# Performance work log

Measured on AMD Instinct MI355X. Metric: run time of the kernel, lower is better.

Reference implementation:

```python
import jax, jax.numpy as jnp
import numpy as np

C, H, W = 32, 64, 64
KH, KW = 5, 5
OH, OW = 60, 60
N_IN = C * H * W
B, S = 64, 4096
CAP = 128


def _build_indices():
    # Enumerate every (c, kh, kw, oh, ow) slot of the unfold, matching
    # fold(unfold(order)) in the torch module (stride 1, pad 0, dilation 1).
    c = np.arange(C)[:, None, None, None, None]
    kh = np.arange(KH)[None, :, None, None, None]
    kw = np.arange(KW)[None, None, :, None, None]
    oh = np.arange(OH)[None, None, None, :, None]
    ow = np.arange(OW)[None, None, None, None, :]
    ids = c * (H * W) + (oh + kh) * W + (ow + kw)          # input flat id feeding slot
    ckk = c * (KH * KW) + kh * KW + kw                     # kernel-local channel index
    j = ckk * (OH * OW) + oh * OW + ow                     # flat slot in order_convoled
    ids, j = np.broadcast_arrays(ids, j)
    ids = ids.ravel().astype(np.int64)
    j = j.ravel().astype(np.int64)
    perm = np.argsort(ids, kind='stable')
    sid, sj = ids[perm], j[perm]
    counts = np.bincount(ids, minlength=N_IN)
    Lmax = int(counts.max())                               # = 25 here
    starts = np.concatenate([[0], np.cumsum(counts)[:-1]])
    rank = np.arange(sid.shape[0]) - starts[sid]
    indices = np.full((N_IN, Lmax), -1, dtype=np.int32)
    indices[sid, rank] = sj
    return indices


def setup_inputs() -> dict:
    key = jax.random.key(0)
    spikes = jax.random.randint(key, (B, S, 1, 1), 0, N_IN, dtype=jnp.int32)
    indices = jnp.asarray(_build_indices())
    return {"spikes": spikes, "indices": indices, "out_h": OH, "out_w": OW, "cap": CAP}


def reference(spikes, indices, out_h, out_w, cap):
    Bn, Sn = spikes.shape[0], spikes.shape[1]
    L = indices.shape[1]
    nbins = out_h * out_w
    E = Sn * L                                             # events per batch element

    ids = spikes[:, :, 0, 0]                               # [B,S] flat input ids
    g = indices[ids]                                       # [B,S,L] slots, -1 padded
    valid = g >= 0
    j = jnp.where(valid, g, 0)
    bins = (j % nbins).reshape(Bn * E)                     # output bin (oh*out_w+ow)
    ckk = (j // nbins).reshape(Bn * E)                     # kernel-local index to store
    valid_f = valid.reshape(Bn * E)
    b_idx = jnp.repeat(jnp.arange(Bn, dtype=jnp.int32), E)

    # Arrival-order rank within each (batch, bin): stable sort by global bin,
    # then rank = position - segment start (running max of change points).
    gbin = jnp.where(valid_f, b_idx * nbins + bins, Bn * nbins)   # sentinel for invalid
    perm = jnp.argsort(gbin)                               # stable
    sorted_gbin = gbin[perm]
    pos = jnp.arange(Bn * E, dtype=jnp.int32)
    change = jnp.concatenate([jnp.ones((1,), bool), sorted_gbin[1:] != sorted_gbin[:-1]])
    seg_start = jax.lax.cummax(jnp.where(change, pos, 0))
    rank_sorted = pos - seg_start
    rank = jnp.zeros(Bn * E, jnp.int32).at[perm].set(rank_sorted)  # inverse perm

    # Scatter ckk into per-bin slots; invalid / overflow events go to slot=cap (dropped).
    slot = jnp.where(valid_f & (rank < cap), rank, cap)
    out = jnp.full((Bn, cap + 1, nbins), -1, dtype=spikes.dtype)
    out = out.at[b_idx, slot, bins].set(jnp.where(valid_f, ckk, -1), mode='drop')
    return out[:, :cap].reshape(Bn, cap, out_h, out_w)
```

## Files before the change

### kernel.cpp

```cpp
#include <hip/hip_runtime.h>

#define OHh   60
#define OWw   60
#define NBINS (OHh * OWw)
#define NB    64
#define NS    4096
#define CAP   128

#define NW     4
#define SEG    (NS / NW)
#define CH     (SEG / 64)
#define WSLOTS 40
#define PRE0   64

__global__ __launch_bounds__(256) void sort_spikes_row4(
    const int* __restrict__ spikes, int* __restrict__ out) {
    const int bid  = (int)blockIdx.x;
    const int b    = bid & (NB - 1);
    const int row  = bid >> 6;
    const int tid  = (int)threadIdx.x;
    const int wv   = tid >> 6;
    const int lane = tid & 63;
    const bool valid  = lane < OWw;
    const int  lane_c = valid ? lane : 127;

    __shared__ short          stage[NW][WSLOTS + 1][64];
    __shared__ unsigned short hits[NW][64];
    __shared__ int            cnt[NW][64];
    __shared__ int            ovf;

    if (tid == 0) ovf = 0;

    const int* __restrict__ sp   = spikes + b * NS + wv * SEG;
    int* __restrict__       outb = out + (size_t)b * (CAP * NBINS) + row * OWw;

    int vs[CH];
#pragma unroll
    for (int c = 0; c < CH; ++c) vs[c] = sp[c * 64 + lane];

    unsigned short* const hitbuf      = &hits[wv][0];
    short* const          stage_lane  = &stage[wv][0][lane];
    short* const          stage_dummy = &stage[wv][WSLOTS][lane];

    int count = 0;
#pragma unroll
    for (int c = 0; c < CH; ++c) {
        const int v   = vs[c];
        const int kh  = ((v >> 6) & 63) - row;
        const bool halo = (unsigned)kh < 5u;
        const int w   = v & 63;
        const int A   = (v >> 12) * 25 + kh * 5 + w;
        const unsigned short P = (unsigned short)((w << 10) | A);

        const unsigned long long mask = __ballot(halo);
        const int pos = __builtin_amdgcn_mbcnt_hi(
            (unsigned)(mask >> 32),
            __builtin_amdgcn_mbcnt_lo((unsigned)mask, 0));
        if (halo) hitbuf[pos] = P;
        const int n = __popcll(mask);

        for (int i = 0; i < n; ++i) {
            const int Pj  = (int)hitbuf[i];
            const int kw  = (Pj >> 10) - lane_c;
            const bool inwin = (unsigned)kw < 5u;
            const int val = (Pj & 0x3ff) - lane_c;
            short* a = (inwin & (count < WSLOTS))
                           ? (stage_lane + count * 64)
                           : stage_dummy;
            *a = (short)val;
            count += inwin;
        }

        if (valid) outb[(PRE0 + wv * CH + c) * NBINS + lane] = -1;
    }
    cnt[wv][lane] = count;
    if (__ballot(count > WSLOTS) && lane == 0) ovf = 1;
    __syncthreads();

    if (ovf == 0) {
        if (valid) {
            const int c0 = cnt[0][lane], c1 = cnt[1][lane];
            const int c2 = cnt[2][lane], c3 = cnt[3][lane];
            const int o1 = c0, o2 = c0 + c1, o3 = o2 + c2;
            const int total = o3 + c3;
#pragma unroll 4
            for (int i = 0; i < PRE0 / NW; ++i) {
                const int k = wv * (PRE0 / NW) + i;
                int val = -1;
                if (k < total) {
                    int wsel = 0, base = 0;
                    if (k >= o1) { wsel = 1; base = o1; }
                    if (k >= o2) { wsel = 2; base = o2; }
                    if (k >= o3) { wsel = 3; base = o3; }
                    val = (int)stage[wsel][k - base][lane];
                }
                outb[k * NBINS + lane] = val;
            }
            for (int k = PRE0 + wv; k < total && k < CAP; k += NW) {
                int wsel = 0, base = 0;
                if (k >= o1) { wsel = 1; base = o1; }
                if (k >= o2) { wsel = 2; base = o2; }
                if (k >= o3) { wsel = 3; base = o3; }
                outb[k * NBINS + lane] = (int)stage[wsel][k - base][lane];
            }
        }
    } else if (wv == 0) {
        const int* __restrict__ spf = spikes + b * NS;
        int cc = 0;
        for (int c = 0; c < NS / 64; ++c) {
            const int v = spf[c * 64 + lane];
            const int h = (v >> 6) & 63;
            unsigned long long mask = __ballot((unsigned)(h - row) < 5u);
            while (mask) {
                const int j = (int)__builtin_ctzll(mask);
                mask &= mask - 1;
                const int vj =
                    __builtin_amdgcn_readlane(v, __builtin_amdgcn_readfirstlane(j));
                const int wj  = vj & 63;
                const int khj = ((vj >> 6) & 63) - row;
                const int cj  = vj >> 12;
                const int kw  = wj - lane;
                if (((unsigned)kw < 5u) & valid) {
                    if (cc < CAP)
                        outb[cc * NBINS + lane] = cj * 25 + khj * 5 + kw;
                    ++cc;
                }
            }
        }
        if (valid)
            for (int k = cc; k < CAP; ++k) outb[k * NBINS + lane] = -1;
    }
}

extern "C" void kernel_launch(void* const* d_in, const int* in_sizes, int n_in,
                              void* d_out, int out_size, void* d_ws, size_t ws_size,
                              hipStream_t stream) {
    const int* spikes = (const int*)d_in[0];
    int* out = (int*)d_out;

    dim3 grid(OHh * NB);
    dim3 block(256);
    sort_spikes_row4<<<grid, block, 0, stream>>>(spikes, out);
}
```

Baseline: 148.9 us.

## Accumulate halo hits then scatter to bins with ballot-based match-any ranking

Each wave now collects all halo hits for its segment into a shared buffer first. It then processes them 12 at a time, with each lane taking one (hit, kw) pair, instead of every lane scanning every hit serially per chunk. Per-bin ranks come from a six-ballot match-any over the bin id, and the stage layout becomes bin-major. This cuts the serial per-hit loop by roughly a factor of 12. In exchange it adds a hit-buffer cap with overflow fallback and a smaller per-bin staging capacity, so the slow fallback path may trigger more often.

```diff
diff --git a/kernel.cpp b/kernel.cpp
--- a/kernel.cpp
+++ b/kernel.cpp
@@ -10,8 +10,10 @@
 #define NW     4
 #define SEG    (NS / NW)
 #define CH     (SEG / 64)
-#define WSLOTS 40
+#define WSLOTS 32
 #define PRE0   64
+#define HCAP   176
+#define HSINK  192
 
 __global__ __launch_bounds__(256) void sort_spikes_row4(
     const int* __restrict__ spikes, int* __restrict__ out) {
@@ -21,15 +23,15 @@
     const int tid  = (int)threadIdx.x;
     const int wv   = tid >> 6;
     const int lane = tid & 63;
-    const bool valid  = lane < OWw;
-    const int  lane_c = valid ? lane : 127;
+    const bool valid = lane < OWw;
 
-    __shared__ short          stage[NW][WSLOTS + 1][64];
-    __shared__ unsigned short hits[NW][64];
-    __shared__ int            cnt[NW][64];
-    __shared__ int            ovf;
+    __shared__ short stage[NW][64][WSLOTS + 1];
+    __shared__ __align__(8) unsigned short hits[NW][256];
+    __shared__ int   cnt[NW][64];
+    __shared__ int   ovf;
 
     if (tid == 0) ovf = 0;
+    cnt[wv][lane] = 0;
 
     const int* __restrict__ sp   = spikes + b * NS + wv * SEG;
     int* __restrict__       outb = out + (size_t)b * (CAP * NBINS) + row * OWw;
@@ -38,43 +40,67 @@
 #pragma unroll
     for (int c = 0; c < CH; ++c) vs[c] = sp[c * 64 + lane];
 
-    unsigned short* const hitbuf      = &hits[wv][0];
-    short* const          stage_lane  = &stage[wv][0][lane];
-    short* const          stage_dummy = &stage[wv][WSLOTS][lane];
+    unsigned short* const hitbuf = &hits[wv][0];
+    const int sinkw = HSINK + lane;
 
-    int count = 0;
+    int hbase = 0;
 #pragma unroll
     for (int c = 0; c < CH; ++c) {
-        const int v   = vs[c];
-        const int kh  = ((v >> 6) & 63) - row;
+        const int v  = vs[c];
+        const int kh = ((v >> 6) & 63) - row;
         const bool halo = (unsigned)kh < 5u;
-        const int w   = v & 63;
-        const int A   = (v >> 12) * 25 + kh * 5 + w;
-        const unsigned short P = (unsigned short)((w << 10) | A);
+        const unsigned short P =
+            (unsigned short)(((v & 63) << 8) | ((v >> 12) << 3) | (kh & 7));
 
         const unsigned long long mask = __ballot(halo);
         const int pos = __builtin_amdgcn_mbcnt_hi(
             (unsigned)(mask >> 32),
             __builtin_amdgcn_mbcnt_lo((unsigned)mask, 0));
-        if (halo) hitbuf[pos] = P;
-        const int n = __popcll(mask);
-
-        for (int i = 0; i < n; ++i) {
-            const int Pj  = (int)hitbuf[i];
-            const int kw  = (Pj >> 10) - lane_c;
-            const bool inwin = (unsigned)kw < 5u;
-            const int val = (Pj & 0x3ff) - lane_c;
-            short* a = (inwin & (count < WSLOTS))
-                           ? (stage_lane + count * 64)
-                           : stage_dummy;
-            *a = (short)val;
-            count += inwin;
-        }
+        const int idx = halo ? (hbase + pos) : sinkw;
+        hitbuf[idx] = P;
+        hbase = min(hbase + (int)__popcll(mask), HCAP);
 
         if (valid) outb[(PRE0 + wv * CH + c) * NBINS + lane] = -1;
     }
-    cnt[wv][lane] = count;
-    if (__ballot(count > WSLOTS) && lane == 0) ovf = 1;
+    if (hbase >= HCAP && lane == 0) ovf = 1;
+
+    const int qi  = (lane < 60) ? (lane / 5) : 4096;
+    const int kwc = lane - qi * 5;
+
+    const int n = hbase;
+    short* const stg = &stage[wv][0][0];
+    int*   const cw  = &cnt[wv][0];
+    for (int hb = 0; hb < n; hb += 12) {
+        const int  hidx = hb + qi;
+        const bool hv   = hidx < n;
+        const int  ridx = hv ? hidx : sinkw;
+        const unsigned P = hitbuf[ridx];
+        const int  w    = (int)(P >> 8);
+        const int  bin  = w - kwc;
+        const bool ok   = hv & ((unsigned)bin < 60u);
+        const int  route = ok ? bin : 62;
+        const int  val  = ((int)((P >> 3) & 31)) * 25 + ((int)(P & 7)) * 5 + kwc;
+
+        unsigned long long m = ~0ull;
+#pragma unroll
+        for (int t = 0; t < 6; ++t) {
+            const bool bit = (route >> t) & 1;
+            const unsigned long long bb = __ballot(bit);
+            m &= bit ? bb : ~bb;
+        }
+        const int rank = __builtin_amdgcn_mbcnt_hi(
+            (unsigned)(m >> 32), __builtin_amdgcn_mbcnt_lo((unsigned)m, 0));
+        const int tot  = (int)__popcll(m);
+        const int base = cw[route];
+        const int slot = min(base + rank, WSLOTS);
+        stg[route * (WSLOTS + 1) + slot] = (short)val;
+        if (rank == tot - 1) cw[route] = base + tot;
+    }
+
+    {
+        const int mycnt = cw[lane];
+        if (__ballot(mycnt > WSLOTS) && lane == 0) ovf = 1;
+    }
     __syncthreads();
 
     if (ovf == 0) {
@@ -92,7 +118,7 @@
                     if (k >= o1) { wsel = 1; base = o1; }
                     if (k >= o2) { wsel = 2; base = o2; }
                     if (k >= o3) { wsel = 3; base = o3; }
-                    val = (int)stage[wsel][k - base][lane];
+                    val = (int)stage[wsel][lane][k - base];
                 }
                 outb[k * NBINS + lane] = val;
             }
@@ -101,7 +127,7 @@
                 if (k >= o1) { wsel = 1; base = o1; }
                 if (k >= o2) { wsel = 2; base = o2; }
                 if (k >= o3) { wsel = 3; base = o3; }
-                outb[k * NBINS + lane] = (int)stage[wsel][k - base][lane];
+                outb[k * NBINS + lane] = (int)stage[wsel][lane][k - base];
             }
         }
     } else if (wv == 0) {
```

Result: slower. 277.5 us (+86.3%).

## Process two output rows per block with two waves per row

Applied to the files above, without the earlier changes.

Each block now handles a pair of output rows. Two waves serve each row, and each wave scans half the spike stream (2048 spikes, loaded in two chunks of 16) instead of a quarter. This halves the grid and the number of redundant spike loads, and makes the merge step choose between only two staged buffers. In exchange, each wave has a serial hit-processing chain twice as long, and the fixed 40-slot staging buffer is more likely to overflow into the slow fallback path.

```diff
diff --git a/kernel.cpp b/kernel.cpp
--- a/kernel.cpp
+++ b/kernel.cpp
@@ -8,21 +8,28 @@
 #define CAP   128
 
 #define NW     4
-#define SEG    (NS / NW)
+#define RPB    2
+#define RG     (OHh / RPB)
+#define SEGS   2
+#define SEG    (NS / SEGS)
 #define CH     (SEG / 64)
 #define WSLOTS 40
 #define PRE0   64
 
-__global__ __launch_bounds__(256) void sort_spikes_row4(
+__global__ __launch_bounds__(256) void sort_spikes_rowpair(
     const int* __restrict__ spikes, int* __restrict__ out) {
     const int bid  = (int)blockIdx.x;
     const int b    = bid & (NB - 1);
-    const int row  = bid >> 6;
+    const int rg   = bid >> 6;
     const int tid  = (int)threadIdx.x;
     const int wv   = tid >> 6;
     const int lane = tid & 63;
     const bool valid  = lane < OWw;
     const int  lane_c = valid ? lane : 127;
+
+    const int rsub = wv >> 1;
+    const int seg  = wv & 1;
+    const int row  = rg * RPB + rsub;
 
     __shared__ short          stage[NW][WSLOTS + 1][64];
     __shared__ unsigned short hits[NW][64];
@@ -31,12 +38,8 @@
 
     if (tid == 0) ovf = 0;
 
-    const int* __restrict__ sp   = spikes + b * NS + wv * SEG;
+    const int* __restrict__ sp   = spikes + b * NS + seg * SEG;
     int* __restrict__       outb = out + (size_t)b * (CAP * NBINS) + row * OWw;
-
-    int vs[CH];
-#pragma unroll
-    for (int c = 0; c < CH; ++c) vs[c] = sp[c * 64 + lane];
 
     unsigned short* const hitbuf      = &hits[wv][0];
     short* const          stage_lane  = &stage[wv][0][lane];
@@ -44,34 +47,42 @@
 
     int count = 0;
 #pragma unroll
-    for (int c = 0; c < CH; ++c) {
-        const int v   = vs[c];
-        const int kh  = ((v >> 6) & 63) - row;
-        const bool halo = (unsigned)kh < 5u;
-        const int w   = v & 63;
-        const int A   = (v >> 12) * 25 + kh * 5 + w;
-        const unsigned short P = (unsigned short)((w << 10) | A);
+    for (int half = 0; half < 2; ++half) {
+        int vs[16];
+#pragma unroll
+        for (int c = 0; c < 16; ++c) vs[c] = sp[(half * 16 + c) * 64 + lane];
 
-        const unsigned long long mask = __ballot(halo);
-        const int pos = __builtin_amdgcn_mbcnt_hi(
-            (unsigned)(mask >> 32),
-            __builtin_amdgcn_mbcnt_lo((unsigned)mask, 0));
-        if (halo) hitbuf[pos] = P;
-        const int n = __popcll(mask);
+#pragma unroll
+        for (int c = 0; c < 16; ++c) {
+            const int cc  = half * 16 + c;
+            const int v   = vs[c];
+            const int kh  = ((v >> 6) & 63) - row;
+            const bool halo = (unsigned)kh < 5u;
+            const int w   = v & 63;
+            const int A   = (v >> 12) * 25 + kh * 5 + w;
+            const unsigned short P = (unsigned short)((w << 10) | A);
 
-        for (int i = 0; i < n; ++i) {
-            const int Pj  = (int)hitbuf[i];
-            const int kw  = (Pj >> 10) - lane_c;
-            const bool inwin = (unsigned)kw < 5u;
-            const int val = (Pj & 0x3ff) - lane_c;
-            short* a = (inwin & (count < WSLOTS))
-                           ? (stage_lane + count * 64)
-                           : stage_dummy;
-            *a = (short)val;
-            count += inwin;
+            const unsigned long long mask = __ballot(halo);
+            const int pos = __builtin_amdgcn_mbcnt_hi(
+                (unsigned)(mask >> 32),
+                __builtin_amdgcn_mbcnt_lo((unsigned)mask, 0));
+            if (halo) hitbuf[pos] = P;
+            const int n = __popcll(mask);
+
+            for (int i = 0; i < n; ++i) {
+                const int Pj  = (int)hitbuf[i];
+                const int kw  = (Pj >> 10) - lane_c;
+                const bool inwin = (unsigned)kw < 5u;
+                const int val = (Pj & 0x3ff) - lane_c;
+                short* a = (inwin & (count < WSLOTS))
+                               ? (stage_lane + count * 64)
+                               : stage_dummy;
+                *a = (short)val;
+                count += inwin;
+            }
+
+            if (valid) outb[(PRE0 + seg * CH + cc) * NBINS + lane] = -1;
         }
-
-        if (valid) outb[(PRE0 + wv * CH + c) * NBINS + lane] = -1;
     }
     cnt[wv][lane] = count;
     if (__ballot(count > WSLOTS) && lane == 0) ovf = 1;
@@ -79,32 +90,28 @@
 
     if (ovf == 0) {
         if (valid) {
-            const int c0 = cnt[0][lane], c1 = cnt[1][lane];
-            const int c2 = cnt[2][lane], c3 = cnt[3][lane];
-            const int o1 = c0, o2 = c0 + c1, o3 = o2 + c2;
-            const int total = o3 + c3;
+            const int w0 = rsub * SEGS;
+            const int c0 = cnt[w0][lane], c1 = cnt[w0 + 1][lane];
+            const int total = c0 + c1;
+            const int kbase = seg * 32;
 #pragma unroll 4
-            for (int i = 0; i < PRE0 / NW; ++i) {
-                const int k = wv * (PRE0 / NW) + i;
+            for (int i = 0; i < 32; ++i) {
+                const int k = kbase + i;
                 int val = -1;
                 if (k < total) {
-                    int wsel = 0, base = 0;
-                    if (k >= o1) { wsel = 1; base = o1; }
-                    if (k >= o2) { wsel = 2; base = o2; }
-                    if (k >= o3) { wsel = 3; base = o3; }
+                    const int wsel = (k >= c0) ? (w0 + 1) : w0;
+                    const int base = (k >= c0) ? c0 : 0;
                     val = (int)stage[wsel][k - base][lane];
                 }
                 outb[k * NBINS + lane] = val;
             }
-            for (int k = PRE0 + wv; k < total && k < CAP; k += NW) {
-                int wsel = 0, base = 0;
-                if (k >= o1) { wsel = 1; base = o1; }
-                if (k >= o2) { wsel = 2; base = o2; }
-                if (k >= o3) { wsel = 3; base = o3; }
+            for (int k = PRE0 + seg; k < total && k < CAP; k += SEGS) {
+                const int wsel = (k >= c0) ? (w0 + 1) : w0;
+                const int base = (k >= c0) ? c0 : 0;
                 outb[k * NBINS + lane] = (int)stage[wsel][k - base][lane];
             }
         }
-    } else if (wv == 0) {
+    } else if (seg == 0) {
         const int* __restrict__ spf = spikes + b * NS;
         int cc = 0;
         for (int c = 0; c < NS / 64; ++c) {
@@ -138,7 +145,7 @@
     const int* spikes = (const int*)d_in[0];
     int* out = (int*)d_out;
 
-    dim3 grid(OHh * NB);
+    dim3 grid(RG * NB);
     dim3 block(256);
-    sort_spikes_row4<<<grid, block, 0, stream>>>(spikes, out);
+    sort_spikes_rowpair<<<grid, block, 0, stream>>>(spikes, out);
 }
```

Result: slower. 153.6 us (+3.1%).

## Replace per-hit lane broadcast loop with atomic presence bitmasks per bin

Applied to the files above, without the earlier changes.

Each wave now appends all halo hits to a shared buffer with up to 160 entries, instead of replaying every hit across all lanes. Lanes are grouped so that each group of five scatters one hit's five kernel-width taps into per-bin presence bitmasks using shared-memory atomicOr, twelve hits per pass. Each bin then walks its own bitmask in arrival order and writes into a shared output image, which is copied out to global memory in coalesced rows. The aim is to cut the serial n-iteration loop that every lane ran per chunk. In exchange the kernel adds LDS atomics, an extra block barrier and a larger shared footprint, and the bitmask walk is divergent across lanes.

```diff
diff --git a/kernel.cpp b/kernel.cpp
--- a/kernel.cpp
+++ b/kernel.cpp
@@ -10,7 +10,7 @@
 #define NW     4
 #define SEG    (NS / NW)
 #define CH     (SEG / 64)
-#define WSLOTS 40
+#define HCAP   160
 #define PRE0   64
 
 __global__ __launch_bounds__(256) void sort_spikes_row4(
@@ -21,15 +21,22 @@
     const int tid  = (int)threadIdx.x;
     const int wv   = tid >> 6;
     const int lane = tid & 63;
-    const bool valid  = lane < OWw;
-    const int  lane_c = valid ? lane : 127;
+    const bool valid = lane < OWw;
 
-    __shared__ short          stage[NW][WSLOTS + 1][64];
-    __shared__ unsigned short hits[NW][64];
+    __shared__ int            hitbuf[NW][256];
+    __shared__ unsigned       pres[NW][64][7];
+    __shared__ unsigned short outimg[PRE0][OWw];
     __shared__ int            cnt[NW][64];
     __shared__ int            ovf;
 
     if (tid == 0) ovf = 0;
+#pragma unroll
+    for (int i = 0; i < 5; ++i) pres[wv][lane][i] = 0u;
+
+    {
+        int* oi = (int*)&outimg[0][0];
+        for (int i = tid; i < PRE0 * OWw / 2; i += 256) oi[i] = -1;
+    }
 
     const int* __restrict__ sp   = spikes + b * NS + wv * SEG;
     int* __restrict__       outb = out + (size_t)b * (CAP * NBINS) + row * OWw;
@@ -38,70 +45,75 @@
 #pragma unroll
     for (int c = 0; c < CH; ++c) vs[c] = sp[c * 64 + lane];
 
-    unsigned short* const hitbuf      = &hits[wv][0];
-    short* const          stage_lane  = &stage[wv][0][lane];
-    short* const          stage_dummy = &stage[wv][WSLOTS][lane];
+    int* const hb_w = &hitbuf[wv][0];
+    const int row5 = row * 5;
 
-    int count = 0;
+    int hbase = 0;
 #pragma unroll
     for (int c = 0; c < CH; ++c) {
-        const int v   = vs[c];
-        const int kh  = ((v >> 6) & 63) - row;
-        const bool halo = (unsigned)kh < 5u;
-        const int w   = v & 63;
-        const int A   = (v >> 12) * 25 + kh * 5 + w;
-        const unsigned short P = (unsigned short)((w << 10) | A);
+        const int v = vs[c];
+        const int h = (v >> 6) & 63;
+        const int w = v & 63;
+        const int A = (v >> 12) * 25 + h * 5 + w - row5;
+        const int R = (w << 16) | A;
+        const bool halo = (unsigned)(h - row) < 5u;
 
         const unsigned long long mask = __ballot(halo);
         const int pos = __builtin_amdgcn_mbcnt_hi(
             (unsigned)(mask >> 32),
             __builtin_amdgcn_mbcnt_lo((unsigned)mask, 0));
-        if (halo) hitbuf[pos] = P;
-        const int n = __popcll(mask);
-
-        for (int i = 0; i < n; ++i) {
-            const int Pj  = (int)hitbuf[i];
-            const int kw  = (Pj >> 10) - lane_c;
-            const bool inwin = (unsigned)kw < 5u;
-            const int val = (Pj & 0x3ff) - lane_c;
-            short* a = (inwin & (count < WSLOTS))
-                           ? (stage_lane + count * 64)
-                           : stage_dummy;
-            *a = (short)val;
-            count += inwin;
-        }
+        if (halo) hb_w[min(hbase + pos, 255)] = R;
+        hbase += (int)__popcll(mask);
 
         if (valid) outb[(PRE0 + wv * CH + c) * NBINS + lane] = -1;
     }
-    cnt[wv][lane] = count;
-    if (__ballot(count > WSLOTS) && lane == 0) ovf = 1;
+    if (hbase > HCAP && lane == 0) ovf = 1;
+    const int n = min(hbase, HCAP);
+
+    const int qi  = (lane < OWw) ? (lane / 5) : 4096;
+    const int kwc = lane - qi * 5;
+    for (int hbi = 0; hbi < n; hbi += 12) {
+        const int hidx = hbi + qi;
+        const int R    = hb_w[min(hidx, 255)];
+        const int bin  = (R >> 16) - kwc;
+        if (((unsigned)bin < 60u) && (hidx < n)) {
+            atomicOr(&pres[wv][bin][hidx >> 5], 1u << (hidx & 31));
+        }
+    }
+
+    unsigned m0 = pres[wv][lane][0], m1 = pres[wv][lane][1];
+    unsigned m2 = pres[wv][lane][2], m3 = pres[wv][lane][3];
+    unsigned m4 = pres[wv][lane][4];
+    cnt[wv][lane] = __builtin_popcount(m0) + __builtin_popcount(m1) +
+                    __builtin_popcount(m2) + __builtin_popcount(m3) +
+                    __builtin_popcount(m4);
     __syncthreads();
 
     if (ovf == 0) {
         if (valid) {
-            const int c0 = cnt[0][lane], c1 = cnt[1][lane];
-            const int c2 = cnt[2][lane], c3 = cnt[3][lane];
-            const int o1 = c0, o2 = c0 + c1, o3 = o2 + c2;
-            const int total = o3 + c3;
+            int k = 0;
+            for (int w = 0; w < wv; ++w) k += cnt[w][lane];
+            unsigned mw[5] = {m0, m1, m2, m3, m4};
+#pragma unroll
+            for (int wd = 0; wd < 5; ++wd) {
+                unsigned mm = mw[wd];
+                while (mm) {
+                    const int j = __builtin_ctz(mm);
+                    mm &= mm - 1;
+                    const int src = wd * 32 + j;
+                    const int ck  = (hb_w[src] & 0xffff) - lane;
+                    if (k < PRE0) outimg[k][lane] = (unsigned short)ck;
+                    else if (k < CAP) outb[k * NBINS + lane] = ck;
+                    ++k;
+                }
+            }
+        }
+        __syncthreads();
+        if (valid) {
 #pragma unroll 4
             for (int i = 0; i < PRE0 / NW; ++i) {
-                const int k = wv * (PRE0 / NW) + i;
-                int val = -1;
-                if (k < total) {
-                    int wsel = 0, base = 0;
-                    if (k >= o1) { wsel = 1; base = o1; }
-                    if (k >= o2) { wsel = 2; base = o2; }
-                    if (k >= o3) { wsel = 3; base = o3; }
-                    val = (int)stage[wsel][k - base][lane];
-                }
-                outb[k * NBINS + lane] = val;
-            }
-            for (int k = PRE0 + wv; k < total && k < CAP; k += NW) {
-                int wsel = 0, base = 0;
-                if (k >= o1) { wsel = 1; base = o1; }
-                if (k >= o2) { wsel = 2; base = o2; }
-                if (k >= o3) { wsel = 3; base = o3; }
-                outb[k * NBINS + lane] = (int)stage[wsel][k - base][lane];
+                const int kk = wv * (PRE0 / NW) + i;
+                outb[kk * NBINS + lane] = (int)(short)outimg[kk][lane];
             }
         }
     } else if (wv == 0) {
```

New measurement: 138.4 us, median of 2. 1.08x faster.
